# Kernel tuning notes

Measured on AMD Instinct MI355X. Metric: run time of the kernel, lower is better.

The kernel has to match this reference:

```python
import jax, jax.numpy as jnp
import numpy as np

R_CHK, N_VAR, BATCH, ITERS, NLEV, ROW_DEG = 144, 576, 512, 3, 16, 15


def setup_inputs() -> dict:
    key = jax.random.key(0)
    rng = np.random.default_rng(0)
    Hnp = np.zeros((R_CHK, N_VAR), np.float32)
    cols = np.argsort(rng.random((R_CHK, N_VAR)), axis=1)[:, :ROW_DEG]
    Hnp[np.arange(R_CHK)[:, None], cols] = 1.0
    H = jnp.asarray(Hnp)
    r = jax.random.normal(key, (BATCH, N_VAR), jnp.float32) * 2.0  # channel LLRs
    alpha = jnp.full((ITERS,), 0.7, jnp.float32)
    beta = jnp.full((ITERS,), 0.05, jnp.float32)
    eta = jnp.full((ITERS,), 0.7, jnp.float32)
    qk = jnp.linspace(-4.0, 4.0, NLEV).astype(jnp.float32)  # learned codebook
    return {"r": r, "alpha": alpha, "beta": beta, "eta": eta, "qk": qk, "H": H}


def _c_to_v(M, alpha, beta, Hb):
    # Normalized offset min-sum check-node update, excluding self-message.
    mag = jnp.where(Hb, jnp.abs(M), jnp.inf)              # [B,R,C]
    two = -jax.lax.top_k(-mag, 2)[0]                      # two smallest per row
    m1, m2 = two[..., 0:1], two[..., 1:2]
    min_excl = jnp.where(mag == m1, m2, m1)               # min over other edges
    sgn = jnp.where(Hb, jnp.sign(M), 1.0)
    row_sign = jnp.prod(sgn, axis=-1, keepdims=True)
    E = alpha * row_sign * sgn * jnp.maximum(min_excl - beta, 0.0)
    return jnp.where(Hb, E, 0.0)


def _quantize(x, eta, qk):
    # Nearest-level lookup in sorted codebook qk, applied to eta*x.
    bnd = 0.5 * (qk[:-1] + qk[1:])                        # [NLEV-1] midpoints
    idx = jnp.searchsorted(bnd, eta * x)
    return qk[idx]


def _decode(r, alpha, beta, eta, qk, H):
    Hb = H > 0.5                                          # [R,C] edge mask
    M = H[None] * r[:, None, :]                           # initial_M: [B,R,C]
    E = jnp.zeros_like(M)
    for it in range(ITERS):
        E = _c_to_v(M, alpha[it], beta[it], Hb)
        E = _quantize(E, eta[it], qk) * H                 # Q on check messages
        col = jnp.sum(E, axis=1, keepdims=True)           # [B,1,C]
        M = H[None] * (r[:, None, :] + col - E)           # update_M (extrinsic)
        M = _quantize(M, eta[it], qk) * H                 # Q on var messages
    return r + jnp.sum(E, axis=1)                         # [B,C]


def reference(r, alpha, beta, eta, qk, H):
    return _decode(r, alpha, beta, eta, qk, H)
```

## Files before the change

### kernel.cpp

```cpp
#include <hip/hip_runtime.h>
#include <hip/hip_bf16.h>
#include <math.h>

#define R_CHK   144
#define N_VAR   576
#define BATCH   512
#define ITERS   3
#define NLEV    16
#define ROW_DEG 15
#define N_EDGE  (R_CHK * ROW_DEG)
#define NWORDS  9
#define DEG_PAD 16

__launch_bounds__(64)
__global__ void k1_bitmask(const float* __restrict__ H,
                           unsigned long long* __restrict__ bits,
                           int* __restrict__ edge_cols) {
    const int i    = blockIdx.x;
    const int lane = threadIdx.x;

    float h[NWORDS];
#pragma unroll
    for (int s = 0; s < NWORDS; ++s) h[s] = H[i * N_VAR + s * 64 + lane];

    unsigned long long m[NWORDS];
#pragma unroll
    for (int s = 0; s < NWORDS; ++s) m[s] = __ballot(h[s] > 0.5f);

#pragma unroll
    for (int s = 0; s < NWORDS; ++s)
        if (lane == s) bits[i * NWORDS + s] = m[s];

    if (lane == 0) {
        int k = 0;
#pragma unroll
        for (int s = 0; s < NWORDS; ++s) {
            unsigned long long mm = m[s];
            while (mm) {
                int b = __ffsll((long long)mm) - 1;
                if (k < ROW_DEG) edge_cols[i * ROW_DEG + k] = s * 64 + b;
                ++k;
                mm &= mm - 1;
            }
        }
    }
}

__launch_bounds__(N_VAR)
__global__ void k2_coltab(const unsigned long long* __restrict__ bits,
                          int* __restrict__ col_edge) {
    __shared__ unsigned long long sb[R_CHK * NWORDS];
    __shared__ int spref[R_CHK * NWORDS];

    const int t = threadIdx.x;

    for (int e = t; e < R_CHK * NWORDS; e += N_VAR) sb[e] = bits[e];
    __syncthreads();

    for (int idx = t; idx < R_CHK * NWORDS; idx += N_VAR) {
        int i = idx / NWORDS, w = idx % NWORDS;
        int p = 0;
        for (int u = 0; u < w; ++u) p += __popcll(sb[i * NWORDS + u]);
        spref[idx] = p;
    }
    __syncthreads();

    const int w   = t >> 6;
    const int bit = t & 63;
    const unsigned long long vmask   = 1ull << bit;
    const unsigned long long lowmask = vmask - 1ull;
    int n = 0;
    for (int i0 = 0; i0 < R_CHK; i0 += 16) {
        unsigned long long mw[16];
        int pf[16];
#pragma unroll
        for (int j = 0; j < 16; ++j) {
            mw[j] = sb[(i0 + j) * NWORDS + w];
            pf[j] = spref[(i0 + j) * NWORDS + w];
        }
#pragma unroll
        for (int j = 0; j < 16; ++j) {
            if (mw[j] & vmask) {
                int rank = pf[j] + __popcll(mw[j] & lowmask);
                if (n < DEG_PAD) col_edge[t * DEG_PAD + n] = (i0 + j) * ROW_DEG + rank;
                ++n;
            }
        }
    }
    for (int j = n; j < DEG_PAD; ++j) col_edge[t * DEG_PAD + j] = N_EDGE;
}

__launch_bounds__(256)
__global__ void decode_kernel(const float* __restrict__ r,
                              const float* __restrict__ alpha,
                              const float* __restrict__ beta,
                              const float* __restrict__ eta,
                              const float* __restrict__ qk,
                              const int* __restrict__ edge_cols,
                              const int* __restrict__ col_edge,
                              float* __restrict__ out) {
    __shared__ float sE[N_EDGE + 1];
    __shared__ float sr[N_VAR];
    __shared__ float st[N_VAR];

    const int b = blockIdx.x;
    const int t = threadIdx.x;

    const float qv = qk[t & 15];
    float bnd[NLEV - 1];
#pragma unroll
    for (int j = 0; j < NLEV - 1; ++j) bnd[j] = 0.5f * (qk[j] + qk[j + 1]);

    float av[ITERS], bv[ITERS], ev[ITERS];
#pragma unroll
    for (int i = 0; i < ITERS; ++i) { av[i] = alpha[i]; bv[i] = beta[i]; ev[i] = eta[i]; }

    int ce0[DEG_PAD], ce1[DEG_PAD], ce2[DEG_PAD];
#pragma unroll
    for (int j = 0; j < DEG_PAD; ++j) ce0[j] = col_edge[t * DEG_PAD + j];
#pragma unroll
    for (int j = 0; j < DEG_PAD; ++j) ce1[j] = col_edge[(t + 256) * DEG_PAD + j];
    if (t < N_VAR - 512) {
#pragma unroll
        for (int j = 0; j < DEG_PAD; ++j) ce2[j] = col_edge[(t + 512) * DEG_PAD + j];
    }

    const bool isrow = (t < R_CHK);
    int cols[ROW_DEG];
    if (isrow) {
#pragma unroll
        for (int k = 0; k < ROW_DEG; ++k) cols[k] = edge_cols[t * ROW_DEG + k];
    }

    for (int v = t; v < N_VAR; v += 256) sr[v] = r[b * N_VAR + v];
    if (t == 0) sE[N_EDGE] = 0.0f;
    __syncthreads();

    float M[ROW_DEG], Eq[ROW_DEG];
    if (isrow) {
#pragma unroll
        for (int k = 0; k < ROW_DEG; ++k) M[k] = sr[cols[k]];
    }

#pragma unroll
    for (int it = 0; it < ITERS; ++it) {
        const float a   = av[it];
        const float bta = bv[it];
        const float et  = ev[it];

        if (isrow) {
            if (it > 0) {
                const float etp = ev[it - 1];
#pragma unroll
                for (int k = 0; k < ROW_DEG; ++k) {
                    float x = st[cols[k]] - Eq[k];
                    float y = etp * x;
                    int idx = 0;
#pragma unroll
                    for (int j = 0; j < NLEV - 1; ++j) idx += (y > bnd[j]) ? 1 : 0;
                    M[k] = __shfl(qv, idx);
                }
            }

            float sg[ROW_DEG];
#pragma unroll
            for (int k = 0; k < ROW_DEG; ++k)
                sg[k] = (M[k] > 0.0f) ? 1.0f : ((M[k] < 0.0f) ? -1.0f : 0.0f);
            float q0 = sg[0] * sg[1],  q1 = sg[2] * sg[3];
            float q2 = sg[4] * sg[5],  q3 = sg[6] * sg[7];
            float q4 = sg[8] * sg[9],  q5 = sg[10] * sg[11];
            float q6 = sg[12] * sg[13], q7 = sg[14];
            float r0 = q0 * q1, r1 = q2 * q3, r2 = q4 * q5, r3 = q6 * q7;
            const float prod = (r0 * r1) * (r2 * r3);

            float a1[8], a2[8];
#pragma unroll
            for (int k = 0; k < 7; ++k) {
                float x = fabsf(M[2 * k]), y = fabsf(M[2 * k + 1]);
                a1[k] = fminf(x, y); a2[k] = fmaxf(x, y);
            }
            a1[7] = fabsf(M[14]); a2[7] = INFINITY;
#pragma unroll
            for (int s = 4; s >= 1; s >>= 1) {
#pragma unroll
                for (int k = 0; k < 4; ++k) {
                    if (k < s) {
                        float lo = fminf(a1[k], a1[k + s]);
                        float hi = fminf(fmaxf(a1[k], a1[k + s]), fminf(a2[k], a2[k + s]));
                        a1[k] = lo; a2[k] = hi;
                    }
                }
            }
            const float m1 = a1[0], m2 = a2[0];

            const float ap = a * prod;
#pragma unroll
            for (int k = 0; k < ROW_DEG; ++k) {
                float ab = fabsf(M[k]);
                float mexcl = (ab == m1) ? m2 : m1;
                float E = (ap * sg[k]) * fmaxf(mexcl - bta, 0.0f);
                float y = et * E;
                int idx = 0;
#pragma unroll
                for (int j = 0; j < NLEV - 1; ++j) idx += (y > bnd[j]) ? 1 : 0;
                float eq = __shfl(qv, idx);
                Eq[k] = eq;
                sE[t * ROW_DEG + k] = eq;
            }
        }
        __syncthreads();

        {
            float s0 = 0.0f, s1 = 0.0f, s2 = 0.0f;
#pragma unroll
            for (int j = 0; j < DEG_PAD; ++j) s0 += sE[ce0[j]];
#pragma unroll
            for (int j = 0; j < DEG_PAD; ++j) s1 += sE[ce1[j]];
            if (t < N_VAR - 512) {
#pragma unroll
                for (int j = 0; j < DEG_PAD; ++j) s2 += sE[ce2[j]];
            }
            float t0 = sr[t] + s0;
            float t1 = sr[t + 256] + s1;
            st[t] = t0;
            st[t + 256] = t1;
            float t2 = 0.0f;
            if (t < N_VAR - 512) {
                t2 = sr[t + 512] + s2;
                st[t + 512] = t2;
            }
            if (it == ITERS - 1) {
                out[b * N_VAR + t] = t0;
                out[b * N_VAR + t + 256] = t1;
                if (t < N_VAR - 512) out[b * N_VAR + t + 512] = t2;
            }
        }
        if (it < ITERS - 1) __syncthreads();
    }
}

extern "C" void kernel_launch(void* const* d_in, const int* in_sizes, int n_in,
                              void* d_out, int out_size, void* d_ws, size_t ws_size,
                              hipStream_t stream) {
    const float* r     = (const float*)d_in[0];
    const float* alpha = (const float*)d_in[1];
    const float* beta  = (const float*)d_in[2];
    const float* eta   = (const float*)d_in[3];
    const float* qk    = (const float*)d_in[4];
    const float* H     = (const float*)d_in[5];
    float* out = (float*)d_out;

    unsigned long long* bits = (unsigned long long*)d_ws;
    int* edge_cols = (int*)(bits + R_CHK * NWORDS);
    int* col_edge  = edge_cols + N_EDGE;

    k1_bitmask<<<R_CHK, 64, 0, stream>>>(H, bits, edge_cols);
    k2_coltab<<<1, N_VAR, 0, stream>>>(bits, col_edge);
    decode_kernel<<<BATCH, 256, 0, stream>>>(r, alpha, beta, eta, qk,
                                             edge_cols, col_edge, out);
}
```

Measured before the change: 42.97 us.

## Decode each codeword with a single wavefront and precompute per-row quantized messages

The decode kernel shrinks from 256 threads to one 64-lane wavefront per codeword. Each lane handles up to three check rows and nine variable columns, and block-level __syncthreads are replaced by wave barriers. The check-message quantization is no longer done per edge: the four possible outputs (±m1, ±m2) are quantized once per row, then selected per edge. The codebook lookup also moves from a shuffle to a register select chain. Per-lane serial work and register pressure rise, which may limit latency hiding, in exchange for removing block synchronization and redundant quantization.

```diff
diff --git a/kernel.cpp b/kernel.cpp
--- a/kernel.cpp
+++ b/kernel.cpp
@@ -11,6 +11,8 @@
 #define N_EDGE  (R_CHK * ROW_DEG)
 #define NWORDS  9
 #define DEG_PAD 16
+#define NCOLP   9
+#define NROWP   3
 
 __launch_bounds__(64)
 __global__ void k1_bitmask(const float* __restrict__ H,
@@ -90,12 +92,12 @@
     for (int j = n; j < DEG_PAD; ++j) col_edge[t * DEG_PAD + j] = N_EDGE;
 }
 
-__launch_bounds__(256)
+__launch_bounds__(64, 1)
 __global__ void decode_kernel(const float* __restrict__ r,
                               const float* __restrict__ alpha,
                               const float* __restrict__ beta,
                               const float* __restrict__ eta,
-                              const float* __restrict__ qk,
+                              const float* __restrict__ qkg,
                               const int* __restrict__ edge_cols,
                               const int* __restrict__ col_edge,
                               float* __restrict__ out) {
@@ -103,139 +105,154 @@
     __shared__ float sr[N_VAR];
     __shared__ float st[N_VAR];
 
-    const int b = blockIdx.x;
-    const int t = threadIdx.x;
-
-    const float qv = qk[t & 15];
-    float bnd[NLEV - 1];
+    const int b    = blockIdx.x;
+    const int lane = threadIdx.x;
+
+    float qk[NLEV], bnd[NLEV - 1];
+#pragma unroll
+    for (int j = 0; j < NLEV; ++j) qk[j] = qkg[j];
 #pragma unroll
     for (int j = 0; j < NLEV - 1; ++j) bnd[j] = 0.5f * (qk[j] + qk[j + 1]);
 
+    auto QZ = [&](float y) -> float {
+        float q = qk[0];
+#pragma unroll
+        for (int j = 0; j < NLEV - 1; ++j) q = (y > bnd[j]) ? qk[j + 1] : q;
+        return q;
+    };
+    const float q0 = QZ(0.0f);
+
     float av[ITERS], bv[ITERS], ev[ITERS];
 #pragma unroll
     for (int i = 0; i < ITERS; ++i) { av[i] = alpha[i]; bv[i] = beta[i]; ev[i] = eta[i]; }
 
-    int ce0[DEG_PAD], ce1[DEG_PAD], ce2[DEG_PAD];
-#pragma unroll
-    for (int j = 0; j < DEG_PAD; ++j) ce0[j] = col_edge[t * DEG_PAD + j];
-#pragma unroll
-    for (int j = 0; j < DEG_PAD; ++j) ce1[j] = col_edge[(t + 256) * DEG_PAD + j];
-    if (t < N_VAR - 512) {
-#pragma unroll
-        for (int j = 0; j < DEG_PAD; ++j) ce2[j] = col_edge[(t + 512) * DEG_PAD + j];
-    }
-
-    const bool isrow = (t < R_CHK);
-    int cols[ROW_DEG];
-    if (isrow) {
-#pragma unroll
-        for (int k = 0; k < ROW_DEG; ++k) cols[k] = edge_cols[t * ROW_DEG + k];
-    }
-
-    for (int v = t; v < N_VAR; v += 256) sr[v] = r[b * N_VAR + v];
-    if (t == 0) sE[N_EDGE] = 0.0f;
-    __syncthreads();
-
-    float M[ROW_DEG], Eq[ROW_DEG];
-    if (isrow) {
-#pragma unroll
-        for (int k = 0; k < ROW_DEG; ++k) M[k] = sr[cols[k]];
+    int ce[NCOLP][DEG_PAD];
+#pragma unroll
+    for (int c = 0; c < NCOLP; ++c) {
+        const int4* p4 = (const int4*)(col_edge + (lane + 64 * c) * DEG_PAD);
+#pragma unroll
+        for (int j = 0; j < 4; ++j) {
+            int4 v = p4[j];
+            ce[c][4 * j + 0] = v.x; ce[c][4 * j + 1] = v.y;
+            ce[c][4 * j + 2] = v.z; ce[c][4 * j + 3] = v.w;
+        }
+    }
+
+    int cols[NROWP][ROW_DEG];
+#pragma unroll
+    for (int p = 0; p < NROWP; ++p) {
+        const int row = lane + 64 * p;
+        if (row < R_CHK) {
+#pragma unroll
+            for (int k = 0; k < ROW_DEG; ++k) cols[p][k] = edge_cols[row * ROW_DEG + k];
+        }
+    }
+
+    float rv[NCOLP];
+#pragma unroll
+    for (int c = 0; c < NCOLP; ++c) {
+        rv[c] = r[b * N_VAR + lane + 64 * c];
+        sr[lane + 64 * c] = rv[c];
+    }
+    if (lane == 0) sE[N_EDGE] = 0.0f;
+    __builtin_amdgcn_wave_barrier();
+
+    float M[NROWP][ROW_DEG], Eq[NROWP][ROW_DEG];
+#pragma unroll
+    for (int p = 0; p < NROWP; ++p) {
+        const int row = lane + 64 * p;
+        if (row < R_CHK) {
+#pragma unroll
+            for (int k = 0; k < ROW_DEG; ++k) M[p][k] = sr[cols[p][k]];
+        }
     }
 
 #pragma unroll
     for (int it = 0; it < ITERS; ++it) {
-        const float a   = av[it];
-        const float bta = bv[it];
-        const float et  = ev[it];
-
-        if (isrow) {
-            if (it > 0) {
-                const float etp = ev[it - 1];
+        const float a = av[it], bta = bv[it], et = ev[it];
+
+        if (it > 0) {
+            const float etp = ev[it - 1];
+#pragma unroll
+            for (int p = 0; p < NROWP; ++p) {
+                const int row = lane + 64 * p;
+                if (row < R_CHK) {
+#pragma unroll
+                    for (int k = 0; k < ROW_DEG; ++k) {
+                        float x = st[cols[p][k]] - Eq[p][k];
+                        M[p][k] = QZ(etp * x);
+                    }
+                }
+            }
+        }
+
+#pragma unroll
+        for (int p = 0; p < NROWP; ++p) {
+            const int row = lane + 64 * p;
+            if (row < R_CHK) {
+                float sg[ROW_DEG];
+#pragma unroll
+                for (int k = 0; k < ROW_DEG; ++k)
+                    sg[k] = (M[p][k] > 0.0f) ? 1.0f : ((M[p][k] < 0.0f) ? -1.0f : 0.0f);
+                float t0 = sg[0] * sg[1],  t1 = sg[2] * sg[3];
+                float t2 = sg[4] * sg[5],  t3 = sg[6] * sg[7];
+                float t4 = sg[8] * sg[9],  t5 = sg[10] * sg[11];
+                float t6 = sg[12] * sg[13], t7 = sg[14];
+                float u0 = t0 * t1, u1 = t2 * t3, u2 = t4 * t5, u3 = t6 * t7;
+                const float prod = (u0 * u1) * (u2 * u3);
+
+                float a1[8], a2[8];
+#pragma unroll
+                for (int k = 0; k < 7; ++k) {
+                    float x = fabsf(M[p][2 * k]), y = fabsf(M[p][2 * k + 1]);
+                    a1[k] = fminf(x, y); a2[k] = fmaxf(x, y);
+                }
+                a1[7] = fabsf(M[p][14]); a2[7] = INFINITY;
+#pragma unroll
+                for (int s = 4; s >= 1; s >>= 1) {
+#pragma unroll
+                    for (int k = 0; k < 4; ++k) {
+                        if (k < s) {
+                            float lo = fminf(a1[k], a1[k + s]);
+                            float hi = fminf(fmaxf(a1[k], a1[k + s]), fminf(a2[k], a2[k + s]));
+                            a1[k] = lo; a2[k] = hi;
+                        }
+                    }
+                }
+                const float m1 = a1[0], m2 = a2[0];
+
+                const float ap = a * prod;
+                const float g1 = fmaxf(m1 - bta, 0.0f);
+                const float g2 = fmaxf(m2 - bta, 0.0f);
+                const float y1 = et * (ap * g1);
+                const float y2 = et * (ap * g2);
+                const float c1p = QZ(y1), c1m = QZ(-y1);
+                const float c2p = QZ(y2), c2m = QZ(-y2);
+
 #pragma unroll
                 for (int k = 0; k < ROW_DEG; ++k) {
-                    float x = st[cols[k]] - Eq[k];
-                    float y = etp * x;
-                    int idx = 0;
-#pragma unroll
-                    for (int j = 0; j < NLEV - 1; ++j) idx += (y > bnd[j]) ? 1 : 0;
-                    M[k] = __shfl(qv, idx);
-                }
-            }
-
-            float sg[ROW_DEG];
-#pragma unroll
-            for (int k = 0; k < ROW_DEG; ++k)
-                sg[k] = (M[k] > 0.0f) ? 1.0f : ((M[k] < 0.0f) ? -1.0f : 0.0f);
-            float q0 = sg[0] * sg[1],  q1 = sg[2] * sg[3];
-            float q2 = sg[4] * sg[5],  q3 = sg[6] * sg[7];
-            float q4 = sg[8] * sg[9],  q5 = sg[10] * sg[11];
-            float q6 = sg[12] * sg[13], q7 = sg[14];
-            float r0 = q0 * q1, r1 = q2 * q3, r2 = q4 * q5, r3 = q6 * q7;
-            const float prod = (r0 * r1) * (r2 * r3);
-
-            float a1[8], a2[8];
-#pragma unroll
-            for (int k = 0; k < 7; ++k) {
-                float x = fabsf(M[2 * k]), y = fabsf(M[2 * k + 1]);
-                a1[k] = fminf(x, y); a2[k] = fmaxf(x, y);
-            }
-            a1[7] = fabsf(M[14]); a2[7] = INFINITY;
-#pragma unroll
-            for (int s = 4; s >= 1; s >>= 1) {
-#pragma unroll
-                for (int k = 0; k < 4; ++k) {
-                    if (k < s) {
-                        float lo = fminf(a1[k], a1[k + s]);
-                        float hi = fminf(fmaxf(a1[k], a1[k + s]), fminf(a2[k], a2[k + s]));
-                        a1[k] = lo; a2[k] = hi;
-                    }
-                }
-            }
-            const float m1 = a1[0], m2 = a2[0];
-
-            const float ap = a * prod;
-#pragma unroll
-            for (int k = 0; k < ROW_DEG; ++k) {
-                float ab = fabsf(M[k]);
-                float mexcl = (ab == m1) ? m2 : m1;
-                float E = (ap * sg[k]) * fmaxf(mexcl - bta, 0.0f);
-                float y = et * E;
-                int idx = 0;
-#pragma unroll
-                for (int j = 0; j < NLEV - 1; ++j) idx += (y > bnd[j]) ? 1 : 0;
-                float eq = __shfl(qv, idx);
-                Eq[k] = eq;
-                sE[t * ROW_DEG + k] = eq;
-            }
-        }
-        __syncthreads();
-
-        {
-            float s0 = 0.0f, s1 = 0.0f, s2 = 0.0f;
-#pragma unroll
-            for (int j = 0; j < DEG_PAD; ++j) s0 += sE[ce0[j]];
-#pragma unroll
-            for (int j = 0; j < DEG_PAD; ++j) s1 += sE[ce1[j]];
-            if (t < N_VAR - 512) {
-#pragma unroll
-                for (int j = 0; j < DEG_PAD; ++j) s2 += sE[ce2[j]];
-            }
-            float t0 = sr[t] + s0;
-            float t1 = sr[t + 256] + s1;
-            st[t] = t0;
-            st[t + 256] = t1;
-            float t2 = 0.0f;
-            if (t < N_VAR - 512) {
-                t2 = sr[t + 512] + s2;
-                st[t + 512] = t2;
-            }
-            if (it == ITERS - 1) {
-                out[b * N_VAR + t] = t0;
-                out[b * N_VAR + t + 256] = t1;
-                if (t < N_VAR - 512) out[b * N_VAR + t + 512] = t2;
-            }
-        }
-        if (it < ITERS - 1) __syncthreads();
+                    const bool ismin = (fabsf(M[p][k]) == m1);
+                    float cp = ismin ? c2p : c1p;
+                    float cm = ismin ? c2m : c1m;
+                    float q = (sg[k] > 0.0f) ? cp : cm;
+                    q = (sg[k] == 0.0f) ? q0 : q;
+                    Eq[p][k] = q;
+                    sE[row * ROW_DEG + k] = q;
+                }
+            }
+        }
+        __builtin_amdgcn_wave_barrier();
+
+#pragma unroll
+        for (int c = 0; c < NCOLP; ++c) {
+            float s = 0.0f;
+#pragma unroll
+            for (int j = 0; j < DEG_PAD; ++j) s += sE[ce[c][j]];
+            const float stv = rv[c] + s;
+            st[lane + 64 * c] = stv;
+            if (it == ITERS - 1) out[b * N_VAR + lane + 64 * c] = stv;
+        }
+        __builtin_amdgcn_wave_barrier();
     }
 }
 
@@ -256,6 +273,6 @@
 
     k1_bitmask<<<R_CHK, 64, 0, stream>>>(H, bits, edge_cols);
     k2_coltab<<<1, N_VAR, 0, stream>>>(bits, col_edge);
-    decode_kernel<<<BATCH, 256, 0, stream>>>(r, alpha, beta, eta, qk,
-                                             edge_cols, col_edge, out);
-}
+    decode_kernel<<<BATCH, 64, 0, stream>>>(r, alpha, beta, eta, qk,
+                                            edge_cols, col_edge, out);
+}
```

Result: slower. 58.66 us (+36.5%).

## Fuse H bitmask and column-table construction into decode kernel, quantize per-row candidates

Applied to the files above, without the earlier changes.

The three launches become one kernel. Each block now rebuilds the H bitmask, its row edge lists and the column-to-edge table in shared memory, which removes two serialized launches, including a single-block kernel. In exchange every block reads the full H matrix (about 330 KB) and redundantly does the table build. The check-node quantization is also cut to four lookups per row, one per sign and minimum case, instead of one per edge. r is kept in registers rather than a shared copy.

```diff
diff --git a/kernel.cpp b/kernel.cpp
--- a/kernel.cpp
+++ b/kernel.cpp
@@ -11,142 +11,143 @@
 #define N_EDGE  (R_CHK * ROW_DEG)
 #define NWORDS  9
 #define DEG_PAD 16
-
-__launch_bounds__(64)
-__global__ void k1_bitmask(const float* __restrict__ H,
-                           unsigned long long* __restrict__ bits,
-                           int* __restrict__ edge_cols) {
-    const int i    = blockIdx.x;
-    const int lane = threadIdx.x;
-
-    float h[NWORDS];
-#pragma unroll
-    for (int s = 0; s < NWORDS; ++s) h[s] = H[i * N_VAR + s * 64 + lane];
-
-    unsigned long long m[NWORDS];
-#pragma unroll
-    for (int s = 0; s < NWORDS; ++s) m[s] = __ballot(h[s] > 0.5f);
-
-#pragma unroll
-    for (int s = 0; s < NWORDS; ++s)
-        if (lane == s) bits[i * NWORDS + s] = m[s];
-
-    if (lane == 0) {
-        int k = 0;
-#pragma unroll
-        for (int s = 0; s < NWORDS; ++s) {
-            unsigned long long mm = m[s];
-            while (mm) {
-                int b = __ffsll((long long)mm) - 1;
-                if (k < ROW_DEG) edge_cols[i * ROW_DEG + k] = s * 64 + b;
-                ++k;
-                mm &= mm - 1;
-            }
-        }
-    }
-}
-
-__launch_bounds__(N_VAR)
-__global__ void k2_coltab(const unsigned long long* __restrict__ bits,
-                          int* __restrict__ col_edge) {
-    __shared__ unsigned long long sb[R_CHK * NWORDS];
-    __shared__ int spref[R_CHK * NWORDS];
-
-    const int t = threadIdx.x;
-
-    for (int e = t; e < R_CHK * NWORDS; e += N_VAR) sb[e] = bits[e];
+#define NPAIR   (R_CHK * NWORDS)
+#define CH      27
+
+__launch_bounds__(256)
+__global__ void fused_decode(const float* __restrict__ r,
+                             const float* __restrict__ alpha,
+                             const float* __restrict__ beta,
+                             const float* __restrict__ eta,
+                             const float* __restrict__ qkg,
+                             const float* __restrict__ H,
+                             float* __restrict__ out) {
+    __shared__ unsigned long long sb[NPAIR];
+    __shared__ int spref[NPAIR];
+    __shared__ unsigned short scr[256][DEG_PAD];
+    __shared__ float sE[N_EDGE + 1];
+    __shared__ float st[N_VAR];
+
+    const int b    = blockIdx.x;
+    const int t    = threadIdx.x;
+    const int w    = t >> 6;
+    const int lane = t & 63;
+
+    const float rv0 = r[b * N_VAR + t];
+    const float rv1 = r[b * N_VAR + t + 256];
+    const float rv2 = (t < 64) ? r[b * N_VAR + t + 512] : 0.0f;
+
+    const float qv = qkg[t & 15];
+    float bnd[NLEV - 1];
+#pragma unroll
+    for (int j = 0; j < NLEV - 1; ++j) bnd[j] = 0.5f * (qkg[j] + qkg[j + 1]);
+    auto QI = [&](float y) -> int {
+        int idx = 0;
+#pragma unroll
+        for (int j = 0; j < NLEV - 1; ++j) idx += (y > bnd[j]) ? 1 : 0;
+        return idx;
+    };
+
+    float av[ITERS], bv[ITERS], ev[ITERS];
+#pragma unroll
+    for (int i = 0; i < ITERS; ++i) { av[i] = alpha[i]; bv[i] = beta[i]; ev[i] = eta[i]; }
+
+    for (int c0 = 0; c0 < 324; c0 += CH) {
+        float h[CH];
+#pragma unroll
+        for (int j = 0; j < CH; ++j) {
+            int q = w + 4 * (c0 + j);
+            h[j] = H[(q / NWORDS) * N_VAR + (q % NWORDS) * 64 + lane];
+        }
+#pragma unroll
+        for (int j = 0; j < CH; ++j) {
+            int q = w + 4 * (c0 + j);
+            unsigned long long m = __ballot(h[j] > 0.5f);
+            if (lane == 0) sb[q] = m;
+        }
+    }
     __syncthreads();
-
-    for (int idx = t; idx < R_CHK * NWORDS; idx += N_VAR) {
-        int i = idx / NWORDS, w = idx % NWORDS;
-        int p = 0;
-        for (int u = 0; u < w; ++u) p += __popcll(sb[i * NWORDS + u]);
-        spref[idx] = p;
-    }
-    __syncthreads();
-
-    const int w   = t >> 6;
-    const int bit = t & 63;
-    const unsigned long long vmask   = 1ull << bit;
-    const unsigned long long lowmask = vmask - 1ull;
-    int n = 0;
-    for (int i0 = 0; i0 < R_CHK; i0 += 16) {
-        unsigned long long mw[16];
-        int pf[16];
-#pragma unroll
-        for (int j = 0; j < 16; ++j) {
-            mw[j] = sb[(i0 + j) * NWORDS + w];
-            pf[j] = spref[(i0 + j) * NWORDS + w];
-        }
-#pragma unroll
-        for (int j = 0; j < 16; ++j) {
-            if (mw[j] & vmask) {
-                int rank = pf[j] + __popcll(mw[j] & lowmask);
-                if (n < DEG_PAD) col_edge[t * DEG_PAD + n] = (i0 + j) * ROW_DEG + rank;
-                ++n;
-            }
-        }
-    }
-    for (int j = n; j < DEG_PAD; ++j) col_edge[t * DEG_PAD + j] = N_EDGE;
-}
-
-__launch_bounds__(256)
-__global__ void decode_kernel(const float* __restrict__ r,
-                              const float* __restrict__ alpha,
-                              const float* __restrict__ beta,
-                              const float* __restrict__ eta,
-                              const float* __restrict__ qk,
-                              const int* __restrict__ edge_cols,
-                              const int* __restrict__ col_edge,
-                              float* __restrict__ out) {
-    __shared__ float sE[N_EDGE + 1];
-    __shared__ float sr[N_VAR];
-    __shared__ float st[N_VAR];
-
-    const int b = blockIdx.x;
-    const int t = threadIdx.x;
-
-    const float qv = qk[t & 15];
-    float bnd[NLEV - 1];
-#pragma unroll
-    for (int j = 0; j < NLEV - 1; ++j) bnd[j] = 0.5f * (qk[j] + qk[j + 1]);
-
-    float av[ITERS], bv[ITERS], ev[ITERS];
-#pragma unroll
-    for (int i = 0; i < ITERS; ++i) { av[i] = alpha[i]; bv[i] = beta[i]; ev[i] = eta[i]; }
-
-    int ce0[DEG_PAD], ce1[DEG_PAD], ce2[DEG_PAD];
-#pragma unroll
-    for (int j = 0; j < DEG_PAD; ++j) ce0[j] = col_edge[t * DEG_PAD + j];
-#pragma unroll
-    for (int j = 0; j < DEG_PAD; ++j) ce1[j] = col_edge[(t + 256) * DEG_PAD + j];
-    if (t < N_VAR - 512) {
-#pragma unroll
-        for (int j = 0; j < DEG_PAD; ++j) ce2[j] = col_edge[(t + 512) * DEG_PAD + j];
-    }
 
     const bool isrow = (t < R_CHK);
     int cols[ROW_DEG];
     if (isrow) {
-#pragma unroll
-        for (int k = 0; k < ROW_DEG; ++k) cols[k] = edge_cols[t * ROW_DEG + k];
-    }
-
-    for (int v = t; v < N_VAR; v += 256) sr[v] = r[b * N_VAR + v];
+        int p = 0;
+#pragma unroll
+        for (int s = 0; s < NWORDS; ++s) {
+            spref[t * NWORDS + s] = p;
+            p += __popcll(sb[t * NWORDS + s]);
+        }
+        int widx = 0;
+        unsigned long long m = sb[t * NWORDS];
+#pragma unroll
+        for (int j = 0; j < ROW_DEG; ++j) {
+            while (m == 0ull) { ++widx; m = sb[t * NWORDS + widx]; }
+            cols[j] = widx * 64 + (__ffsll((long long)m) - 1);
+            m &= m - 1;
+        }
+    }
+    __syncthreads();
+
+    int ce0[DEG_PAD], ce1[DEG_PAD], ce2[DEG_PAD];
+#pragma unroll
+    for (int cc = 0; cc < 3; ++cc) {
+        const int c = t + 256 * cc;
+        if (c < N_VAR) {
+            const int wq  = c >> 6;
+            const int bit = c & 63;
+            const unsigned long long vmask = 1ull << bit;
+            const unsigned long long lowm  = vmask - 1ull;
+            int n = 0;
+            for (int i0 = 0; i0 < R_CHK; i0 += 16) {
+                unsigned long long mw[16];
+                int pf[16];
+#pragma unroll
+                for (int j = 0; j < 16; ++j) {
+                    mw[j] = sb[(i0 + j) * NWORDS + wq];
+                    pf[j] = spref[(i0 + j) * NWORDS + wq];
+                }
+#pragma unroll
+                for (int j = 0; j < 16; ++j) {
+                    if (mw[j] & vmask) {
+                        int rank = pf[j] + __popcll(mw[j] & lowm);
+                        if (n < DEG_PAD)
+                            scr[t][n] = (unsigned short)((i0 + j) * ROW_DEG + rank);
+                        ++n;
+                    }
+                }
+            }
+            for (int j = (n < DEG_PAD ? n : DEG_PAD); j < DEG_PAD; ++j)
+                scr[t][j] = (unsigned short)N_EDGE;
+            if (cc == 0) {
+#pragma unroll
+                for (int j = 0; j < DEG_PAD; ++j) ce0[j] = scr[t][j];
+            } else if (cc == 1) {
+#pragma unroll
+                for (int j = 0; j < DEG_PAD; ++j) ce1[j] = scr[t][j];
+            } else {
+#pragma unroll
+                for (int j = 0; j < DEG_PAD; ++j) ce2[j] = scr[t][j];
+            }
+        }
+    }
+
+    st[t] = rv0;
+    st[t + 256] = rv1;
+    if (t < 64) st[t + 512] = rv2;
     if (t == 0) sE[N_EDGE] = 0.0f;
     __syncthreads();
 
+    const float q0 = __shfl(qv, QI(0.0f));
+
     float M[ROW_DEG], Eq[ROW_DEG];
     if (isrow) {
 #pragma unroll
-        for (int k = 0; k < ROW_DEG; ++k) M[k] = sr[cols[k]];
+        for (int k = 0; k < ROW_DEG; ++k) M[k] = st[cols[k]];
     }
 
 #pragma unroll
     for (int it = 0; it < ITERS; ++it) {
-        const float a   = av[it];
-        const float bta = bv[it];
-        const float et  = ev[it];
+        const float a = av[it], bta = bv[it], et = ev[it];
 
         if (isrow) {
             if (it > 0) {
@@ -154,11 +155,7 @@
 #pragma unroll
                 for (int k = 0; k < ROW_DEG; ++k) {
                     float x = st[cols[k]] - Eq[k];
-                    float y = etp * x;
-                    int idx = 0;
-#pragma unroll
-                    for (int j = 0; j < NLEV - 1; ++j) idx += (y > bnd[j]) ? 1 : 0;
-                    M[k] = __shfl(qv, idx);
+                    M[k] = __shfl(qv, QI(etp * x));
                 }
             }
 
@@ -166,12 +163,12 @@
 #pragma unroll
             for (int k = 0; k < ROW_DEG; ++k)
                 sg[k] = (M[k] > 0.0f) ? 1.0f : ((M[k] < 0.0f) ? -1.0f : 0.0f);
-            float q0 = sg[0] * sg[1],  q1 = sg[2] * sg[3];
-            float q2 = sg[4] * sg[5],  q3 = sg[6] * sg[7];
-            float q4 = sg[8] * sg[9],  q5 = sg[10] * sg[11];
-            float q6 = sg[12] * sg[13], q7 = sg[14];
-            float r0 = q0 * q1, r1 = q2 * q3, r2 = q4 * q5, r3 = q6 * q7;
-            const float prod = (r0 * r1) * (r2 * r3);
+            float t0 = sg[0] * sg[1],  t1 = sg[2] * sg[3];
+            float t2 = sg[4] * sg[5],  t3 = sg[6] * sg[7];
+            float t4 = sg[8] * sg[9],  t5 = sg[10] * sg[11];
+            float t6 = sg[12] * sg[13], t7 = sg[14];
+            float u0 = t0 * t1, u1 = t2 * t3, u2 = t4 * t5, u3 = t6 * t7;
+            const float prod = (u0 * u1) * (u2 * u3);
 
             float a1[8], a2[8];
 #pragma unroll
@@ -194,18 +191,21 @@
             const float m1 = a1[0], m2 = a2[0];
 
             const float ap = a * prod;
+            const float g1 = fmaxf(m1 - bta, 0.0f);
+            const float g2 = fmaxf(m2 - bta, 0.0f);
+            const float y1 = et * (ap * g1);
+            const float y2 = et * (ap * g2);
+            const float c1p = __shfl(qv, QI(y1)), c1m = __shfl(qv, QI(-y1));
+            const float c2p = __shfl(qv, QI(y2)), c2m = __shfl(qv, QI(-y2));
 #pragma unroll
             for (int k = 0; k < ROW_DEG; ++k) {
-                float ab = fabsf(M[k]);
-                float mexcl = (ab == m1) ? m2 : m1;
-                float E = (ap * sg[k]) * fmaxf(mexcl - bta, 0.0f);
-                float y = et * E;
-                int idx = 0;
-#pragma unroll
-                for (int j = 0; j < NLEV - 1; ++j) idx += (y > bnd[j]) ? 1 : 0;
-                float eq = __shfl(qv, idx);
-                Eq[k] = eq;
-                sE[t * ROW_DEG + k] = eq;
+                const bool ismin = (fabsf(M[k]) == m1);
+                float cp = ismin ? c2p : c1p;
+                float cm = ismin ? c2m : c1m;
+                float q = (sg[k] > 0.0f) ? cp : cm;
+                q = (sg[k] == 0.0f) ? q0 : q;
+                Eq[k] = q;
+                sE[t * ROW_DEG + k] = q;
             }
         }
         __syncthreads();
@@ -216,23 +216,20 @@
             for (int j = 0; j < DEG_PAD; ++j) s0 += sE[ce0[j]];
 #pragma unroll
             for (int j = 0; j < DEG_PAD; ++j) s1 += sE[ce1[j]];
-            if (t < N_VAR - 512) {
+            if (t < 64) {
 #pragma unroll
                 for (int j = 0; j < DEG_PAD; ++j) s2 += sE[ce2[j]];
             }
-            float t0 = sr[t] + s0;
-            float t1 = sr[t + 256] + s1;
-            st[t] = t0;
-            st[t + 256] = t1;
-            float t2 = 0.0f;
-            if (t < N_VAR - 512) {
-                t2 = sr[t + 512] + s2;
-                st[t + 512] = t2;
-            }
+            float w0 = rv0 + s0;
+            float w1 = rv1 + s1;
+            st[t] = w0;
+            st[t + 256] = w1;
+            float w2 = 0.0f;
+            if (t < 64) { w2 = rv2 + s2; st[t + 512] = w2; }
             if (it == ITERS - 1) {
-                out[b * N_VAR + t] = t0;
-                out[b * N_VAR + t + 256] = t1;
-                if (t < N_VAR - 512) out[b * N_VAR + t + 512] = t2;
+                out[b * N_VAR + t] = w0;
+                out[b * N_VAR + t + 256] = w1;
+                if (t < 64) out[b * N_VAR + t + 512] = w2;
             }
         }
         if (it < ITERS - 1) __syncthreads();
@@ -250,12 +247,5 @@
     const float* H     = (const float*)d_in[5];
     float* out = (float*)d_out;
 
-    unsigned long long* bits = (unsigned long long*)d_ws;
-    int* edge_cols = (int*)(bits + R_CHK * NWORDS);
-    int* col_edge  = edge_cols + N_EDGE;
-
-    k1_bitmask<<<R_CHK, 64, 0, stream>>>(H, bits, edge_cols);
-    k2_coltab<<<1, N_VAR, 0, stream>>>(bits, col_edge);
-    decode_kernel<<<BATCH, 256, 0, stream>>>(r, alpha, beta, eta, qk,
-                                             edge_cols, col_edge, out);
+    fused_decode<<<BATCH, 256, 0, stream>>>(r, alpha, beta, eta, qk, H, out);
 }
```

New measurement: 71.84 us. +67.2%, slower.
